# Performance work log

Hardware: AMD Instinct MI355X
Metric: run time of the kernel (lower is better)

## Reference

```python
import jax, jax.numpy as jnp
import numpy as np

EPS = 1e-8  # matches torch F.cosine_similarity default eps


def setup_inputs() -> dict:
    key = jax.random.key(0)
    k0, k1, k2, k3 = jax.random.split(key, 4)
    B, S, H, D, E = 8, 128, 768, 256, 50000
    return {
        "hidden_states": jax.random.normal(k0, (B, S, H), dtype=jnp.float32),
        "W": jax.random.normal(k1, (D, H), dtype=jnp.float32) * 0.02,
        "b": jnp.zeros((D,), dtype=jnp.float32),
        "md_W": jax.random.normal(k2, (3, H), dtype=jnp.float32) * 0.02,
        "md_b": jnp.zeros((3,), dtype=jnp.float32),
        "entity_embedding": jax.random.normal(k3, (E, D), dtype=jnp.float32),
    }


def reference(hidden_states, W, b, md_W, md_b, entity_embedding):
    # Mention detection head: linear + log_softmax over dim=1 (seq dim, as in torch code)
    md_logits = jnp.einsum("bsh,ch->bsc", hidden_states, md_W) + md_b  # [B,S,3]
    md_out = jax.nn.log_softmax(md_logits, axis=1)

    # Entity disambiguation head: linear -> tanh -> cosine similarity vs entity table.
    # cosine_similarity(a,b) = <a,b> / (max(||a||,eps) * max(||b||,eps)); expressed as
    # L2-normalize both sides then a single GEMM (mathematically identical, no [B,S,E,D] broadcast).
    proj = jnp.tanh(jnp.einsum("bsh,dh->bsd", hidden_states, W) + b)  # [B,S,D]
    proj_n = proj / jnp.maximum(jnp.linalg.norm(proj, axis=-1, keepdims=True), EPS)
    ent_n = entity_embedding / jnp.maximum(
        jnp.linalg.norm(entity_embedding, axis=-1, keepdims=True), EPS
    )
    similarity = jnp.einsum("bsd,ed->bse", proj_n, ent_n)  # [B,S,E]
    return (md_out, similarity)
```

## Files before the change

kernel.cpp:

```cpp
#include <hip/hip_runtime.h>
#include <cstdint>
#include <cstddef>

#define Bz 8
#define Sz 128
#define Hz 768
#define Dz 256
#define Ez 50000
#define Mz (Bz*Sz)
#define EPAD 50048

#define ENT_BLOCKS  12512
#define CONV_BLOCKS 960
#define MD_BLOCKS   256
#define FRONT_BLOCKS (ENT_BLOCKS + CONV_BLOCKS + MD_BLOCKS)

typedef __bf16 bf16x8 __attribute__((ext_vector_type(8)));
typedef float  f32x4  __attribute__((ext_vector_type(4)));

__device__ __forceinline__ unsigned short f2bf(float f) {
  unsigned int u = __float_as_uint(f);
  u += 0x7fffu + ((u >> 16) & 1u);
  return (unsigned short)(u >> 16);
}

#define GLOAD_LDS16(gp, lp) \
  __builtin_amdgcn_global_load_lds((__attribute__((address_space(1))) void*)(gp), \
                                   (__attribute__((address_space(3))) void*)(lp), 16, 0, 0)

__global__ __launch_bounds__(256) void k_front(
    const float* __restrict__ hid, const float* __restrict__ W,
    const float* __restrict__ mdW, const float* __restrict__ mdb,
    const float* __restrict__ ent,
    ushort4* __restrict__ hb, ushort4* __restrict__ wb,
    ushort4* __restrict__ en, float* __restrict__ lt) {
  const int tid  = threadIdx.x;
  const int lane = tid & 63;
  const int wave = tid >> 6;
  int blk = blockIdx.x;

  if (blk < ENT_BLOCKS) {
    int row = blk * 4 + wave;
    if (row >= Ez) {
      en[(size_t)row*64 + lane] = make_ushort4(0,0,0,0);
      return;
    }
    float4 v = ((const float4*)ent)[(size_t)row*64 + lane];
    float ss = v.x*v.x + v.y*v.y + v.z*v.z + v.w*v.w;
    #pragma unroll
    for (int off = 32; off > 0; off >>= 1) ss += __shfl_xor(ss, off, 64);
    float inv = 1.f / fmaxf(sqrtf(ss), 1e-8f);
    ushort4 o;
    o.x = f2bf(v.x*inv); o.y = f2bf(v.y*inv); o.z = f2bf(v.z*inv); o.w = f2bf(v.w*inv);
    en[(size_t)row*64 + lane] = o;
    return;
  }
  blk -= ENT_BLOCKS;

  if (blk < CONV_BLOCKS) {
    int i = blk * 256 + tid;
    float4 v = (i < 196608) ? ((const float4*)hid)[i] : ((const float4*)W)[i - 196608];
    ushort4 o;
    o.x = f2bf(v.x); o.y = f2bf(v.y); o.z = f2bf(v.z); o.w = f2bf(v.w);
    if (i < 196608) hb[i] = o; else wb[i - 196608] = o;
    return;
  }
  blk -= CONV_BLOCKS;

  int row = blk * 4 + wave;
  const float4* hr = (const float4*)hid + (size_t)row*192 + lane*3;
  float4 a0 = hr[0], a1 = hr[1], a2 = hr[2];
  const float4* w4 = (const float4*)mdW;
  float p[3];
  #pragma unroll
  for (int c = 0; c < 3; ++c) {
    float4 w0 = w4[c*192 + lane*3], w1 = w4[c*192 + lane*3 + 1], w2 = w4[c*192 + lane*3 + 2];
    p[c] = a0.x*w0.x + a0.y*w0.y + a0.z*w0.z + a0.w*w0.w
         + a1.x*w1.x + a1.y*w1.y + a1.z*w1.z + a1.w*w1.w
         + a2.x*w2.x + a2.y*w2.y + a2.z*w2.z + a2.w*w2.w;
  }
  #pragma unroll
  for (int c = 0; c < 3; ++c)
    #pragma unroll
    for (int off = 32; off > 0; off >>= 1) p[c] += __shfl_xor(p[c], off, 64);
  if (lane == 0) {
    #pragma unroll
    for (int c = 0; c < 3; ++c) lt[c*Mz + row] = p[c] + mdb[c];
  }
}

__global__ void k_md_softmax(const float* __restrict__ lt, float* __restrict__ out) {
  int b = blockIdx.x / 3, c = blockIdx.x % 3;
  int s = threadIdx.x;
  float logit = lt[c*Mz + b*Sz + s];
  __shared__ float red[Sz];
  red[s] = logit; __syncthreads();
  for (int off = 64; off > 0; off >>= 1) {
    if (s < off) red[s] = fmaxf(red[s], red[s+off]);
    __syncthreads();
  }
  float mx = red[0]; __syncthreads();
  red[s] = expf(logit - mx); __syncthreads();
  for (int off = 64; off > 0; off >>= 1) {
    if (s < off) red[s] += red[s+off];
    __syncthreads();
  }
  float lse = mx + logf(red[0]);
  out[(size_t)(b*Sz + s)*3 + c] = logit - lse;
}

__global__ __launch_bounds__(256, 1) void k_proj_norm(
    const unsigned short* __restrict__ A,
    const unsigned short* __restrict__ Bm,
    const float* __restrict__ bias,
    unsigned short* __restrict__ Pn) {
  __shared__ unsigned short Alds[32*32];
  __shared__ unsigned short Blds[256*32];
  __shared__ float ssq[32][4];
  const int tid  = threadIdx.x;
  const int lane = tid & 63;
  const int wave = tid >> 6;
  const int m0 = blockIdx.x * 32;
  const int srow   = lane >> 2;
  const int schunk = lane & 3;
  const unsigned short* Agb = A  + (size_t)(m0 + srow)*Hz + schunk*8;
  const unsigned short* Bgb = Bm + (size_t)(wave*64 + srow)*Hz + schunk*8;

  f32x4 acc[2][4];
  f32x4 z = {0.f,0.f,0.f,0.f};
  #pragma unroll
  for (int i = 0; i < 2; ++i)
    #pragma unroll
    for (int j = 0; j < 4; ++j) acc[i][j] = z;

  const int kof = (lane >> 4) * 8;
  const int fr  = lane & 15;

  for (int kt = 0; kt < Hz; kt += 32) {
    if (wave == 0) {
      GLOAD_LDS16(Agb + kt,                 &Alds[0]);
      GLOAD_LDS16(Agb + 16*(size_t)Hz + kt, &Alds[16*32]);
    }
    #pragma unroll
    for (int c = 0; c < 4; ++c)
      GLOAD_LDS16(Bgb + c*16*(size_t)Hz + kt, &Blds[(wave*64 + c*16)*32]);
    __syncthreads();
    bf16x8 af[2], bq[4];
    #pragma unroll
    for (int mi = 0; mi < 2; ++mi)
      af[mi] = *(const bf16x8*)&Alds[(mi*16 + fr)*32 + kof];
    #pragma unroll
    for (int ni = 0; ni < 4; ++ni)
      bq[ni] = *(const bf16x8*)&Blds[(wave*64 + ni*16 + fr)*32 + kof];
    #pragma unroll
    for (int mi = 0; mi < 2; ++mi)
      #pragma unroll
      for (int ni = 0; ni < 4; ++ni)
        acc[mi][ni] = __builtin_amdgcn_mfma_f32_16x16x32_bf16(af[mi], bq[ni], acc[mi][ni], 0, 0, 0);
    __syncthreads();
  }

  const int rl = (lane >> 4) * 4;
  #pragma unroll
  for (int mi = 0; mi < 2; ++mi) {
    #pragma unroll
    for (int reg = 0; reg < 4; ++reg) {
      float s = 0.f;
      #pragma unroll
      for (int ni = 0; ni < 4; ++ni) {
        float v = tanhf(acc[mi][ni][reg] + bias[wave*64 + ni*16 + fr]);
        acc[mi][ni][reg] = v;
        s += v*v;
      }
      s += __shfl_xor(s, 1, 64); s += __shfl_xor(s, 2, 64);
      s += __shfl_xor(s, 4, 64); s += __shfl_xor(s, 8, 64);
      if ((lane & 15) == 0) ssq[mi*16 + rl + reg][wave] = s;
    }
  }
  __syncthreads();
  #pragma unroll
  for (int mi = 0; mi < 2; ++mi) {
    #pragma unroll
    for (int reg = 0; reg < 4; ++reg) {
      int r = mi*16 + rl + reg;
      float inv = 1.f / fmaxf(sqrtf(ssq[r][0] + ssq[r][1] + ssq[r][2] + ssq[r][3]), 1e-8f);
      #pragma unroll
      for (int ni = 0; ni < 4; ++ni)
        Pn[(size_t)(m0 + r)*Dz + wave*64 + ni*16 + fr] = f2bf(acc[mi][ni][reg] * inv);
    }
  }
}

__global__ __launch_bounds__(256) void k_sim(
    const unsigned short* __restrict__ A, const unsigned short* __restrict__ Bm,
    float* __restrict__ C) {
  __shared__ unsigned short Alds[128*32];
  __shared__ unsigned short Blds[128*32];
  const int tid  = threadIdx.x;
  const int lane = tid & 63;
  const int wave = tid >> 6;
  const int w  = (blockIdx.x & 7) * 391 + (blockIdx.x >> 3);
  const int m0 = (w & 7) * 128;
  const int n0 = (w >> 3) * 128;
  const int wm = (wave >> 1) * 64;
  const int wn = (wave & 1) * 64;
  const int srow   = lane >> 2;
  const int schunk = lane & 3;
  const unsigned short* Agb = A  + (size_t)(m0 + wave*32 + srow)*Dz + schunk*8;
  const unsigned short* Bgb = Bm + (size_t)(n0 + wave*32 + srow)*Dz + schunk*8;
  unsigned short* Al0 = &Alds[(wave*32)*32];
  unsigned short* Al1 = &Alds[(wave*32+16)*32];
  unsigned short* Bl0 = &Blds[(wave*32)*32];
  unsigned short* Bl1 = &Blds[(wave*32+16)*32];

  f32x4 acc[4][4];
  f32x4 z = {0.f,0.f,0.f,0.f};
  #pragma unroll
  for (int i = 0; i < 4; ++i)
    #pragma unroll
    for (int j = 0; j < 4; ++j) acc[i][j] = z;

  const int kof = (lane >> 4) * 8;
  const int fr  = lane & 15;

  for (int kt = 0; kt < Dz; kt += 32) {
    GLOAD_LDS16(Agb + kt,                 Al0);
    GLOAD_LDS16(Agb + 16*(size_t)Dz + kt, Al1);
    GLOAD_LDS16(Bgb + kt,                 Bl0);
    GLOAD_LDS16(Bgb + 16*(size_t)Dz + kt, Bl1);
    __syncthreads();
    bf16x8 af[4], bq[4];
    #pragma unroll
    for (int mi = 0; mi < 4; ++mi)
      af[mi] = *(const bf16x8*)&Alds[(wm + mi*16 + fr)*32 + kof];
    #pragma unroll
    for (int ni = 0; ni < 4; ++ni)
      bq[ni] = *(const bf16x8*)&Blds[(wn + ni*16 + fr)*32 + kof];
    #pragma unroll
    for (int mi = 0; mi < 4; ++mi)
      #pragma unroll
      for (int ni = 0; ni < 4; ++ni)
        acc[mi][ni] = __builtin_amdgcn_mfma_f32_16x16x32_bf16(af[mi], bq[ni], acc[mi][ni], 0, 0, 0);
    __syncthreads();
  }

  const int rbase = m0 + wm + (lane >> 4) * 4;
  const int cbase = n0 + wn + (lane & 15);
  #pragma unroll
  for (int mi = 0; mi < 4; ++mi) {
    #pragma unroll
    for (int ni = 0; ni < 4; ++ni) {
      int n = cbase + ni*16;
      if (n < Ez) {
        #pragma unroll
        for (int reg = 0; reg < 4; ++reg) {
          int m = rbase + mi*16 + reg;
          __builtin_nontemporal_store(acc[mi][ni][reg], &C[(size_t)m * Ez + n]);
        }
      }
    }
  }
}

extern "C" void kernel_launch(void* const* d_in, const int* in_sizes, int n_in,
                              void* d_out, int out_size, void* d_ws, size_t ws_size,
                              hipStream_t stream) {
  (void)in_sizes; (void)n_in; (void)out_size; (void)ws_size;
  const float* hid = (const float*)d_in[0];
  const float* W   = (const float*)d_in[1];
  const float* bb  = (const float*)d_in[2];
  const float* mdW = (const float*)d_in[3];
  const float* mdb = (const float*)d_in[4];
  const float* ent = (const float*)d_in[5];
  float* out = (float*)d_out;

  char* ws = (char*)d_ws;
  unsigned short* hb = (unsigned short*)(ws);
  unsigned short* wb = (unsigned short*)(ws + 1572864);
  unsigned short* pn = (unsigned short*)(ws + 1966080);
  float*          lt = (float*)         (ws + 2490368);
  unsigned short* en = (unsigned short*)(ws + 2502656);

  k_front<<<FRONT_BLOCKS, 256, 0, stream>>>(hid, W, mdW, mdb, ent,
                                            (ushort4*)hb, (ushort4*)wb, (ushort4*)en, lt);
  k_md_softmax<<<Bz*3, Sz, 0, stream>>>(lt, out);
  k_proj_norm<<<32, 256, 0, stream>>>(hb, wb, bb, pn);
  k_sim<<<3128, 256, 0, stream>>>(pn, en, out + (size_t)Mz*3);
}
```

Measured before the change: 313.1 us.

## Fuse entity normalization and bf16 conversion into the similarity GEMM

Removes the separate entity-normalization pass from the front kernel. Each similarity block now loads its 128 fp32 entity rows, L2-normalizes them, converts them to bf16 and stores the full-K B tile in XOR-swizzled LDS, so only A is streamed per k-step. This drops the normalized-entity workspace write and read. In exchange, each entity tile is normalized redundantly by all 8 M-tile blocks, which adds up to 8x fp32 entity reads. LDS per block also grows to about 72KB, which lowers occupancy.

```diff
diff --git a/kernel.cpp b/kernel.cpp
--- a/kernel.cpp
+++ b/kernel.cpp
@@ -10,10 +10,9 @@
 #define Mz (Bz*Sz)
 #define EPAD 50048
 
-#define ENT_BLOCKS  12512
 #define CONV_BLOCKS 960
 #define MD_BLOCKS   256
-#define FRONT_BLOCKS (ENT_BLOCKS + CONV_BLOCKS + MD_BLOCKS)
+#define FRONT_BLOCKS (CONV_BLOCKS + MD_BLOCKS)
 
 typedef __bf16 bf16x8 __attribute__((ext_vector_type(8)));
 typedef float  f32x4  __attribute__((ext_vector_type(4)));
@@ -31,31 +30,12 @@
 __global__ __launch_bounds__(256) void k_front(
     const float* __restrict__ hid, const float* __restrict__ W,
     const float* __restrict__ mdW, const float* __restrict__ mdb,
-    const float* __restrict__ ent,
     ushort4* __restrict__ hb, ushort4* __restrict__ wb,
-    ushort4* __restrict__ en, float* __restrict__ lt) {
+    float* __restrict__ lt) {
   const int tid  = threadIdx.x;
   const int lane = tid & 63;
   const int wave = tid >> 6;
   int blk = blockIdx.x;
-
-  if (blk < ENT_BLOCKS) {
-    int row = blk * 4 + wave;
-    if (row >= Ez) {
-      en[(size_t)row*64 + lane] = make_ushort4(0,0,0,0);
-      return;
-    }
-    float4 v = ((const float4*)ent)[(size_t)row*64 + lane];
-    float ss = v.x*v.x + v.y*v.y + v.z*v.z + v.w*v.w;
-    #pragma unroll
-    for (int off = 32; off > 0; off >>= 1) ss += __shfl_xor(ss, off, 64);
-    float inv = 1.f / fmaxf(sqrtf(ss), 1e-8f);
-    ushort4 o;
-    o.x = f2bf(v.x*inv); o.y = f2bf(v.y*inv); o.z = f2bf(v.z*inv); o.w = f2bf(v.w*inv);
-    en[(size_t)row*64 + lane] = o;
-    return;
-  }
-  blk -= ENT_BLOCKS;
 
   if (blk < CONV_BLOCKS) {
     int i = blk * 256 + tid;
@@ -192,10 +172,11 @@
 }
 
 __global__ __launch_bounds__(256) void k_sim(
-    const unsigned short* __restrict__ A, const unsigned short* __restrict__ Bm,
+    const unsigned short* __restrict__ A,
+    const float* __restrict__ ent,
     float* __restrict__ C) {
   __shared__ unsigned short Alds[128*32];
-  __shared__ unsigned short Blds[128*32];
+  __shared__ unsigned short Blds[128*256];
   const int tid  = threadIdx.x;
   const int lane = tid & 63;
   const int wave = tid >> 6;
@@ -206,12 +187,29 @@
   const int wn = (wave & 1) * 64;
   const int srow   = lane >> 2;
   const int schunk = lane & 3;
-  const unsigned short* Agb = A  + (size_t)(m0 + wave*32 + srow)*Dz + schunk*8;
-  const unsigned short* Bgb = Bm + (size_t)(n0 + wave*32 + srow)*Dz + schunk*8;
+  const unsigned short* Agb = A + (size_t)(m0 + wave*32 + srow)*Dz + schunk*8;
   unsigned short* Al0 = &Alds[(wave*32)*32];
   unsigned short* Al1 = &Alds[(wave*32+16)*32];
-  unsigned short* Bl0 = &Blds[(wave*32)*32];
-  unsigned short* Bl1 = &Blds[(wave*32+16)*32];
+
+  {
+    const int r0 = wave * 32;
+    char* bl = (char*)Blds;
+    #pragma unroll 4
+    for (int s = 0; s < 32; ++s) {
+      int r  = r0 + s;
+      int gn = n0 + r;
+      float4 v = make_float4(0.f, 0.f, 0.f, 0.f);
+      if (gn < Ez) v = ((const float4*)ent)[(size_t)gn*64 + lane];
+      float ss = v.x*v.x + v.y*v.y + v.z*v.z + v.w*v.w;
+      #pragma unroll
+      for (int off = 32; off > 0; off >>= 1) ss += __shfl_xor(ss, off, 64);
+      float inv = 1.f / fmaxf(sqrtf(ss), 1e-8f);
+      ushort4 o;
+      o.x = f2bf(v.x*inv); o.y = f2bf(v.y*inv); o.z = f2bf(v.z*inv); o.w = f2bf(v.w*inv);
+      *(ushort4*)(bl + r*512 + ((lane*8) ^ ((r&15)<<4))) = o;
+    }
+  }
+  __syncthreads();
 
   f32x4 acc[4][4];
   f32x4 z = {0.f,0.f,0.f,0.f};
@@ -222,20 +220,21 @@
 
   const int kof = (lane >> 4) * 8;
   const int fr  = lane & 15;
+  const char* blr = (const char*)Blds;
 
   for (int kt = 0; kt < Dz; kt += 32) {
     GLOAD_LDS16(Agb + kt,                 Al0);
     GLOAD_LDS16(Agb + 16*(size_t)Dz + kt, Al1);
-    GLOAD_LDS16(Bgb + kt,                 Bl0);
-    GLOAD_LDS16(Bgb + 16*(size_t)Dz + kt, Bl1);
     __syncthreads();
     bf16x8 af[4], bq[4];
     #pragma unroll
     for (int mi = 0; mi < 4; ++mi)
       af[mi] = *(const bf16x8*)&Alds[(wm + mi*16 + fr)*32 + kof];
     #pragma unroll
-    for (int ni = 0; ni < 4; ++ni)
-      bq[ni] = *(const bf16x8*)&Blds[(wn + ni*16 + fr)*32 + kof];
+    for (int ni = 0; ni < 4; ++ni) {
+      int rr = wn + ni*16 + fr;
+      bq[ni] = *(const bf16x8*)(blr + rr*512 + (((kt + kof)*2) ^ ((rr&15)<<4)));
+    }
     #pragma unroll
     for (int mi = 0; mi < 4; ++mi)
       #pragma unroll
@@ -279,11 +278,10 @@
   unsigned short* wb = (unsigned short*)(ws + 1572864);
   unsigned short* pn = (unsigned short*)(ws + 1966080);
   float*          lt = (float*)         (ws + 2490368);
-  unsigned short* en = (unsigned short*)(ws + 2502656);
-
-  k_front<<<FRONT_BLOCKS, 256, 0, stream>>>(hid, W, mdW, mdb, ent,
-                                            (ushort4*)hb, (ushort4*)wb, (ushort4*)en, lt);
+
+  k_front<<<FRONT_BLOCKS, 256, 0, stream>>>(hid, W, mdW, mdb,
+                                            (ushort4*)hb, (ushort4*)wb, lt);
   k_md_softmax<<<Bz*3, Sz, 0, stream>>>(lt, out);
   k_proj_norm<<<32, 256, 0, stream>>>(hb, wb, bb, pn);
-  k_sim<<<3128, 256, 0, stream>>>(pn, en, out + (size_t)Mz*3);
-}
+  k_sim<<<3128, 256, 0, stream>>>(pn, ent, out + (size_t)Mz*3);
+}
```

Result: slower. 463.4 us (+48.0%).
